# Performance work log

Measured on AMD Instinct MI355X. Metric: run time of the kernel, lower is better.

The kernel has to match this reference:

```python
import jax, jax.numpy as jnp
import numpy as np

V = 25000
E = 100000
NODE_IN = 74
EDGE_IN = 12
OUT = 64
EHID = 128
NUM_STEPS = 6


def setup_inputs() -> dict:
    key = jax.random.key(0)
    ks = jax.random.split(key, 12)
    s = 0.05
    node_feats = jax.random.normal(ks[0], (V, NODE_IN), dtype=jnp.float32)
    edge_feats = jax.random.normal(ks[1], (E, EDGE_IN), dtype=jnp.float32)
    src = jax.random.randint(ks[2], (E,), 0, V)
    dst = jax.random.randint(ks[3], (E,), 0, V)
    # project_node_feats: Linear(node_in, out)
    Wp = jax.random.normal(ks[4], (NODE_IN, OUT), dtype=jnp.float32) * s
    bp = jnp.zeros((OUT,), dtype=jnp.float32)
    # edge network: Linear(edge_in, ehid) -> ReLU -> Linear(ehid, out*out)
    We1 = jax.random.normal(ks[5], (EDGE_IN, EHID), dtype=jnp.float32) * s
    be1 = jnp.zeros((EHID,), dtype=jnp.float32)
    We2 = jax.random.normal(ks[6], (EHID, OUT * OUT), dtype=jnp.float32) * s
    be2 = jnp.zeros((OUT * OUT,), dtype=jnp.float32)
    # NNConv output bias
    bias = jnp.zeros((OUT,), dtype=jnp.float32)
    return {
        "node_feats": node_feats, "edge_feats": edge_feats,
        "src": src, "dst": dst,
        "Wp": Wp, "bp": bp,
        "We1": We1, "be1": be1, "We2": We2, "be2": be2,
        "bias": bias,
    }


def reference(node_feats, edge_feats, src, dst, Wp, bp, We1, be1, We2, be2, bias):
    # project node features
    h = jax.nn.relu(node_feats @ Wp + bp)  # [V, OUT]
    # per-edge weight matrices (same every step -> hoist out of loop)
    ew = jax.nn.relu(edge_feats @ We1 + be1) @ We2 + be2  # [E, OUT*OUT]
    ew = ew.reshape(E, OUT, OUT)
    for _ in range(NUM_STEPS):
        # gather src node feats, batched matvec, scatter-sum to dst
        msg = jnp.einsum('ei,eio->eo', h[src], ew)  # [E, OUT]
        agg = jax.ops.segment_sum(msg, dst, num_segments=V)  # [V, OUT]
        h = jax.nn.relu(agg + bias)
    return h
```

## Files before the change

kernel.cpp:

```cpp
#include <hip/hip_runtime.h>
#include <hip/hip_bf16.h>

#define Vn 25000
#define En 100000
#define NODE_IN 74
#define EDGE_IN 12
#define OUTD 64
#define EHID 128
#define NUM_STEPS 6

#define HPAD 68

typedef __attribute__((ext_vector_type(8))) _Float16 half8;
typedef __attribute__((ext_vector_type(16))) float floatx16;

__global__ void proj_kernel(const float* __restrict__ node,
                            const float* __restrict__ Wp,
                            const float* __restrict__ bp,
                            float* __restrict__ h) {
  __shared__ float nf[NODE_IN];
  int v = blockIdx.x;
  int o = threadIdx.x;
  for (int i = o; i < NODE_IN; i += 64) nf[i] = node[(size_t)v * NODE_IN + i];
  __syncthreads();
  float acc = bp[o];
  for (int i = 0; i < NODE_IN; ++i) acc = fmaf(nf[i], Wp[i * OUTD + o], acc);
  h[(size_t)v * OUTD + o] = fmaxf(acc, 0.0f);
}

__global__ void edge_kernel(const float* __restrict__ ef,
                            const float* __restrict__ We1,
                            const float* __restrict__ be1,
                            _Float16* __restrict__ f) {
  __shared__ float es[EDGE_IN];
  int e = blockIdx.x;
  int k = threadIdx.x;
  if (k < EDGE_IN) es[k] = ef[(size_t)e * EDGE_IN + k];
  __syncthreads();
  float acc = be1[k];
  for (int j = 0; j < EDGE_IN; ++j) acc = fmaf(es[j], We1[j * EHID + k], acc);
  f[(size_t)e * EHID + k] = (_Float16)fmaxf(acc, 0.0f);
}

__global__ void w2r_kernel(const float* __restrict__ We2,
                           _Float16* __restrict__ w2s) {
  int g = blockIdx.x * 256 + threadIdx.x;
  int j = g & 7;
  int lane = (g >> 3) & 63;
  int s = (g >> 9) & 7;
  int c = (g >> 12) & 1;
  int i = g >> 13;
  int k = s * 16 + 8 * (lane >> 5) + j;
  int col = i * 64 + c * 32 + (lane & 31);
  w2s[g] = (_Float16)We2[(size_t)k * (OUTD * OUTD) + col];
}

__global__ __launch_bounds__(256) void msg_kernel(
    const float* __restrict__ h,
    const _Float16* __restrict__ f,
    const _Float16* __restrict__ w2s,
    const int* __restrict__ src,
    const int* __restrict__ dst,
    const float* __restrict__ be2,
    float* __restrict__ agg) {
  __shared__ float h_t[64 * HPAD];
  __shared__ int s_dst[64];

  const int tid = threadIdx.x;
  const int wvq = tid >> 6;
  const int eh = wvq >> 1;
  const int ch = wvq & 1;
  const int lane = tid & 63;
  const int l31 = lane & 31;
  const int lh = lane >> 5;
  const int e0 = blockIdx.x * 64;

  if (tid < 64) {
    int e = e0 + tid;
    s_dst[tid] = (e < En) ? dst[e] : -1;
  }
  {
    int e = tid & 63;
    int ib = tid >> 6;
    int eg = e0 + e;
    int sv = (eg < En) ? src[eg] : 0;
    const float4* hp = reinterpret_cast<const float4*>(h + (size_t)sv * OUTD + ib * 16);
    for (int cc = 0; cc < 4; ++cc) {
      float4 val = hp[cc];
      int i4 = ib * 16 + cc * 4;
      h_t[(i4 + 0) * HPAD + e] = val.x;
      h_t[(i4 + 1) * HPAD + e] = val.y;
      h_t[(i4 + 2) * HPAD + e] = val.z;
      h_t[(i4 + 3) * HPAD + e] = val.w;
    }
  }
  __syncthreads();

  half8 afr[8];
  {
    int e = e0 + eh * 32 + l31;
    if (e >= En) e = En - 1;
    const _Float16* fr = f + (size_t)e * EHID + 8 * lh;
    for (int s = 0; s < 8; ++s)
      afr[s] = *reinterpret_cast<const half8*>(fr + s * 16);
  }

  const _Float16* w2b = w2s + ch * 4096 + lane * 8;

#define LOADB(dstv, ii)                                                     \
  {                                                                         \
    const _Float16* p_ = w2b + (size_t)(ii) * 8192;                         \
    dstv[0] = *reinterpret_cast<const half8*>(p_);                          \
    dstv[1] = *reinterpret_cast<const half8*>(p_ + 512);                    \
    dstv[2] = *reinterpret_cast<const half8*>(p_ + 1024);                   \
    dstv[3] = *reinterpret_cast<const half8*>(p_ + 1536);                   \
    dstv[4] = *reinterpret_cast<const half8*>(p_ + 2048);                   \
    dstv[5] = *reinterpret_cast<const half8*>(p_ + 2560);                   \
    dstv[6] = *reinterpret_cast<const half8*>(p_ + 3072);                   \
    dstv[7] = *reinterpret_cast<const half8*>(p_ + 3584);                   \
  }

  floatx16 acc = (floatx16){0.f};

  half8 ba[8], bb[8];
  LOADB(ba, 0);
  LOADB(bb, 1);

#define BODY(iv, breg)                                                        \
  {                                                                           \
    _Float16 hh = (_Float16)h_t[(iv) * HPAD + eh * 32 + l31];                 \
    half8 hb = (half8){hh, hh, hh, hh, hh, hh, hh, hh};                       \
    for (int s = 0; s < 8; ++s) {                                             \
      half8 as = afr[s] * hb;                                                 \
      acc = __builtin_amdgcn_mfma_f32_32x32x16_f16(as, breg[s], acc, 0, 0, 0); \
    }                                                                         \
  }

  for (int ii = 0; ii < 32; ++ii) {
    int i0 = 2 * ii;
    BODY(i0, ba);
    {
      int inx = (i0 + 2 < 64) ? i0 + 2 : 63;
      LOADB(ba, inx);
    }
    BODY(i0 + 1, bb);
    {
      int inx = (i0 + 3 < 64) ? i0 + 3 : 63;
      LOADB(bb, inx);
    }
  }

  {
    for (int s = 0; s < 4; ++s) {
      half8 ha, b2;
      for (int j = 0; j < 8; ++j) {
        int i = s * 16 + 8 * lh + j;
        ha[j] = (_Float16)h_t[i * HPAD + eh * 32 + l31];
        b2[j] = (_Float16)be2[i * 64 + ch * 32 + l31];
      }
      acc = __builtin_amdgcn_mfma_f32_32x32x16_f16(ha, b2, acc, 0, 0, 0);
    }
  }

  int col = ch * 32 + l31;
  for (int reg = 0; reg < 16; ++reg) {
    int r = (reg & 3) + 8 * (reg >> 2) + 4 * lh;
    int d = s_dst[eh * 32 + r];
    if (d >= 0) atomicAdd(&agg[(size_t)d * OUTD + col], acc[reg]);
  }
}

__global__ void update_kernel(float* __restrict__ agg,
                              const float* __restrict__ bias,
                              float* __restrict__ hout,
                              float* __restrict__ dout, int last) {
  int g = blockIdx.x * 256 + threadIdx.x;
  if (g >= Vn * OUTD) return;
  float v = agg[g];
  agg[g] = 0.0f;
  float r = fmaxf(v + bias[g & 63], 0.0f);
  hout[g] = r;
  if (last) dout[g] = r;
}

extern "C" void kernel_launch(void* const* d_in, const int* in_sizes, int n_in,
                              void* d_out, int out_size, void* d_ws, size_t ws_size,
                              hipStream_t stream) {
  const float* node = (const float*)d_in[0];
  const float* edge = (const float*)d_in[1];
  const int* src = (const int*)d_in[2];
  const int* dst = (const int*)d_in[3];
  const float* Wp   = (const float*)d_in[4];
  const float* bp   = (const float*)d_in[5];
  const float* We1  = (const float*)d_in[6];
  const float* be1  = (const float*)d_in[7];
  const float* We2  = (const float*)d_in[8];
  const float* be2  = (const float*)d_in[9];
  const float* bias = (const float*)d_in[10];
  float* out = (float*)d_out;

  char* ws = (char*)d_ws;
  float* agg = (float*)(ws);
  float* h_a = (float*)(ws + 6400000);
  float* h_b = (float*)(ws + 12800000);
  _Float16* f   = (_Float16*)(ws + 19200000);
  _Float16* w2s = (_Float16*)(ws + 44800000);

  hipMemsetAsync(agg, 0, (size_t)Vn * OUTD * sizeof(float), stream);
  proj_kernel<<<Vn, 64, 0, stream>>>(node, Wp, bp, h_a);
  edge_kernel<<<En, 128, 0, stream>>>(edge, We1, be1, f);
  w2r_kernel<<<(OUTD * OUTD * EHID) / 256, 256, 0, stream>>>(We2, w2s);

  float* hin = h_a;
  float* hout = h_b;
  for (int s = 0; s < NUM_STEPS; ++s) {
    msg_kernel<<<(En + 63) / 64, 256, 0, stream>>>(hin, f, w2s, src, dst, be2, agg);
    update_kernel<<<(Vn * OUTD + 255) / 256, 256, 0, stream>>>(
        agg, bias, hout, out, s == NUM_STEPS - 1);
    float* t = hin; hin = hout; hout = t;
  }
}
```

Before: 990.4 us.

## Split message kernel K dimension across two waves with LDS reduction

Doubles the message kernel block to 512 threads and splits the 128-wide hidden (K) dimension of the MFMA contraction between wave pairs. The second half writes its partial accumulators to shared memory and the first half adds them before the atomic scatter. The gathered node features are also stored in LDS as fp16 instead of fp32. This aims to raise parallelism and cut per-wave register pressure and the serial MFMA chain, at the cost of an extra barrier and 16KB of LDS for the reduction buffer.

```diff
diff --git a/kernel.cpp b/kernel.cpp
--- a/kernel.cpp
+++ b/kernel.cpp
@@ -9,6 +9,7 @@
 #define EHID 128
 #define NUM_STEPS 6
 
+#define EPB 64
 #define HPAD 68
 
 typedef __attribute__((ext_vector_type(8))) _Float16 half8;
@@ -55,7 +56,7 @@
   w2s[g] = (_Float16)We2[(size_t)k * (OUTD * OUTD) + col];
 }
 
-__global__ __launch_bounds__(256) void msg_kernel(
+__global__ __launch_bounds__(512) void msg_kernel(
     const float* __restrict__ h,
     const _Float16* __restrict__ f,
     const _Float16* __restrict__ w2s,
@@ -63,19 +64,21 @@
     const int* __restrict__ dst,
     const float* __restrict__ be2,
     float* __restrict__ agg) {
-  __shared__ float h_t[64 * HPAD];
-  __shared__ int s_dst[64];
+  __shared__ _Float16 h_t[64 * HPAD];
+  __shared__ float accbuf[4 * 1024];
+  __shared__ int s_dst[EPB];
 
   const int tid = threadIdx.x;
   const int wvq = tid >> 6;
-  const int eh = wvq >> 1;
-  const int ch = wvq & 1;
+  const int eh = (wvq >> 2) & 1;
+  const int ch = (wvq >> 1) & 1;
+  const int kh = wvq & 1;
   const int lane = tid & 63;
   const int l31 = lane & 31;
   const int lh = lane >> 5;
-  const int e0 = blockIdx.x * 64;
-
-  if (tid < 64) {
+  const int e0 = blockIdx.x * EPB;
+
+  if (tid < EPB) {
     int e = e0 + tid;
     s_dst[tid] = (e < En) ? dst[e] : -1;
   }
@@ -84,28 +87,28 @@
     int ib = tid >> 6;
     int eg = e0 + e;
     int sv = (eg < En) ? src[eg] : 0;
-    const float4* hp = reinterpret_cast<const float4*>(h + (size_t)sv * OUTD + ib * 16);
-    for (int cc = 0; cc < 4; ++cc) {
+    const float4* hp = reinterpret_cast<const float4*>(h + (size_t)sv * OUTD + ib * 8);
+    for (int cc = 0; cc < 2; ++cc) {
       float4 val = hp[cc];
-      int i4 = ib * 16 + cc * 4;
-      h_t[(i4 + 0) * HPAD + e] = val.x;
-      h_t[(i4 + 1) * HPAD + e] = val.y;
-      h_t[(i4 + 2) * HPAD + e] = val.z;
-      h_t[(i4 + 3) * HPAD + e] = val.w;
-    }
-  }
-  __syncthreads();
-
-  half8 afr[8];
+      int i4 = ib * 8 + cc * 4;
+      h_t[(i4 + 0) * HPAD + e] = (_Float16)val.x;
+      h_t[(i4 + 1) * HPAD + e] = (_Float16)val.y;
+      h_t[(i4 + 2) * HPAD + e] = (_Float16)val.z;
+      h_t[(i4 + 3) * HPAD + e] = (_Float16)val.w;
+    }
+  }
+  __syncthreads();
+
+  half8 afr[4];
   {
     int e = e0 + eh * 32 + l31;
     if (e >= En) e = En - 1;
-    const _Float16* fr = f + (size_t)e * EHID + 8 * lh;
-    for (int s = 0; s < 8; ++s)
+    const _Float16* fr = f + (size_t)e * EHID + kh * 64 + 8 * lh;
+    for (int s = 0; s < 4; ++s)
       afr[s] = *reinterpret_cast<const half8*>(fr + s * 16);
   }
 
-  const _Float16* w2b = w2s + ch * 4096 + lane * 8;
+  const _Float16* w2b = w2s + ch * 4096 + kh * 2048 + lane * 8;
 
 #define LOADB(dstv, ii)                                                     \
   {                                                                         \
@@ -114,23 +117,19 @@
     dstv[1] = *reinterpret_cast<const half8*>(p_ + 512);                    \
     dstv[2] = *reinterpret_cast<const half8*>(p_ + 1024);                   \
     dstv[3] = *reinterpret_cast<const half8*>(p_ + 1536);                   \
-    dstv[4] = *reinterpret_cast<const half8*>(p_ + 2048);                   \
-    dstv[5] = *reinterpret_cast<const half8*>(p_ + 2560);                   \
-    dstv[6] = *reinterpret_cast<const half8*>(p_ + 3072);                   \
-    dstv[7] = *reinterpret_cast<const half8*>(p_ + 3584);                   \
   }
 
   floatx16 acc = (floatx16){0.f};
 
-  half8 ba[8], bb[8];
+  half8 ba[4], bb[4];
   LOADB(ba, 0);
   LOADB(bb, 1);
 
 #define BODY(iv, breg)                                                        \
   {                                                                           \
-    _Float16 hh = (_Float16)h_t[(iv) * HPAD + eh * 32 + l31];                 \
+    _Float16 hh = h_t[(iv) * HPAD + eh * 32 + l31];                           \
     half8 hb = (half8){hh, hh, hh, hh, hh, hh, hh, hh};                       \
-    for (int s = 0; s < 8; ++s) {                                             \
+    for (int s = 0; s < 4; ++s) {                                             \
       half8 as = afr[s] * hb;                                                 \
       acc = __builtin_amdgcn_mfma_f32_32x32x16_f16(as, breg[s], acc, 0, 0, 0); \
     }                                                                         \
@@ -150,23 +149,34 @@
     }
   }
 
-  {
+  if (kh == 0) {
     for (int s = 0; s < 4; ++s) {
       half8 ha, b2;
       for (int j = 0; j < 8; ++j) {
         int i = s * 16 + 8 * lh + j;
-        ha[j] = (_Float16)h_t[i * HPAD + eh * 32 + l31];
+        ha[j] = h_t[i * HPAD + eh * 32 + l31];
         b2[j] = (_Float16)be2[i * 64 + ch * 32 + l31];
       }
       acc = __builtin_amdgcn_mfma_f32_32x32x16_f16(ha, b2, acc, 0, 0, 0);
     }
   }
 
-  int col = ch * 32 + l31;
-  for (int reg = 0; reg < 16; ++reg) {
-    int r = (reg & 3) + 8 * (reg >> 2) + 4 * lh;
-    int d = s_dst[eh * 32 + r];
-    if (d >= 0) atomicAdd(&agg[(size_t)d * OUTD + col], acc[reg]);
+  {
+    float* ab = &accbuf[(eh * 2 + ch) * 1024];
+    if (kh == 1) {
+      for (int reg = 0; reg < 16; ++reg) ab[reg * 64 + lane] = acc[reg];
+    }
+  }
+  __syncthreads();
+  if (kh == 0) {
+    const float* ab = &accbuf[(eh * 2 + ch) * 1024];
+    int col = ch * 32 + l31;
+    for (int reg = 0; reg < 16; ++reg) {
+      float v = acc[reg] + ab[reg * 64 + lane];
+      int r = (reg & 3) + 8 * (reg >> 2) + 4 * lh;
+      int d = s_dst[eh * 32 + r];
+      if (d >= 0) atomicAdd(&agg[(size_t)d * OUTD + col], v);
+    }
   }
 }
 
@@ -214,7 +224,7 @@
   float* hin = h_a;
   float* hout = h_b;
   for (int s = 0; s < NUM_STEPS; ++s) {
-    msg_kernel<<<(En + 63) / 64, 256, 0, stream>>>(hin, f, w2s, src, dst, be2, agg);
+    msg_kernel<<<(En + EPB - 1) / EPB, 512, 0, stream>>>(hin, f, w2s, src, dst, be2, agg);
     update_kernel<<<(Vn * OUTD + 255) / 256, 256, 0, stream>>>(
         agg, bias, hout, out, s == NUM_STEPS - 1);
     float* t = hin; hin = hout; hout = t;
```

After: 1.001 ms. About the same (+1.0%).
